# Kernel tuning notes

Measured on AMD Instinct MI355X. Metric: run time of the kernel, lower is better.

The kernel has to match this reference:

```python
import jax, jax.numpy as jnp
import numpy as np

N_NODES = 50000

def _gcn_norm(edge_index, num_nodes):
    # PyG gcn_norm with add_self_loops=True, edge_weight=1
    src = jnp.concatenate([edge_index[0], jnp.arange(num_nodes, dtype=edge_index.dtype)])
    dst = jnp.concatenate([edge_index[1], jnp.arange(num_nodes, dtype=edge_index.dtype)])
    deg = jax.ops.segment_sum(jnp.ones(src.shape[0], dtype=jnp.float32), dst, num_segments=num_nodes)
    dis = jnp.where(deg > 0, jax.lax.rsqrt(jnp.maximum(deg, 1e-12)), 0.0)
    norm = dis[src] * dis[dst]  # [E+N]
    return src, dst, norm

def _gcn_layer(x, src, dst, norm, W, b, num_nodes):
    # x' = x @ W^T; out_i = sum_{(j->i)} norm_e * x'_j + b
    xw = x @ W.T                      # [N, h]
    msg = xw[src] * norm[:, None]     # [E+N, h] gathered + scaled messages
    out = jax.ops.segment_sum(msg, dst, num_segments=num_nodes)
    return out + b

def setup_inputs() -> dict:
    key = jax.random.key(0)
    k1, k2, k3, k4 = jax.random.split(key, 4)
    h = 128
    E = 600000
    embeddings = jax.random.normal(k1, (N_NODES, h), dtype=jnp.float32)
    edge_index = jax.random.randint(k2, (2, E), 0, N_NODES, dtype=jnp.int64)
    scale = 1.0 / np.sqrt(h)
    W1 = jax.random.normal(k3, (h, h), dtype=jnp.float32) * scale
    W2 = jax.random.normal(k4, (h, h), dtype=jnp.float32) * scale
    b1 = jnp.zeros((h,), dtype=jnp.float32)
    b2 = jnp.zeros((h,), dtype=jnp.float32)
    return {"embeddings": embeddings, "edge_index": edge_index,
            "W1": W1, "b1": b1, "W2": W2, "b2": b2}

def reference(embeddings, edge_index, W1, b1, W2, b2):
    src, dst, norm = _gcn_norm(edge_index, N_NODES)
    x = _gcn_layer(embeddings, src, dst, norm, W1, b1, N_NODES)
    x = _gcn_layer(x, src, dst, norm, W2, b2, N_NODES)
    return x
```

## Files before the change

kernel.cpp:

```cpp
#include <hip/hip_runtime.h>

typedef unsigned short u16;
typedef unsigned int   u32;

#define H    128
#define PAD  64
#define LROW 136
#define MT   16

typedef __attribute__((ext_vector_type(8))) short bf16x8;
typedef __attribute__((ext_vector_type(4))) float f32x4;

__device__ __forceinline__ float bfbits2f(u32 bits16) {
  union { float f; u32 u; } c; c.u = bits16 << 16; return c.f;
}
__device__ __forceinline__ u16 f2bf(float f) {
  union { float f; u32 u; } c; c.f = f;
  u32 u = c.u;
  return (u16)((u + 0x7fffu + ((u >> 16) & 1u)) >> 16);
}
__device__ __forceinline__ u32 fbits(float f) {
  union { float f; u32 u; } c; c.f = f; return c.u;
}

__device__ __forceinline__ void acc8(float* a, uint4 v) {
  a[0] += bfbits2f(v.x & 0xffffu); a[1] += bfbits2f(v.x >> 16);
  a[2] += bfbits2f(v.y & 0xffffu); a[3] += bfbits2f(v.y >> 16);
  a[4] += bfbits2f(v.z & 0xffffu); a[5] += bfbits2f(v.z >> 16);
  a[6] += bfbits2f(v.w & 0xffffu); a[7] += bfbits2f(v.w >> 16);
}

__global__ void k_init(int* __restrict__ cnt, int N,
                       const float* __restrict__ W1, u16* __restrict__ W1h, u16* __restrict__ W1l,
                       const float* __restrict__ W2, u16* __restrict__ W2h, u16* __restrict__ W2l) {
  int i = blockIdx.x * blockDim.x + threadIdx.x;
  if (i < N) cnt[i] = 0;
  if (i < H * H) {
    float w1 = W1[i];
    u16 h1 = f2bf(w1);
    W1h[i] = h1; W1l[i] = f2bf(w1 - bfbits2f(h1));
    float w2 = W2[i];
    u16 h2 = f2bf(w2);
    W2h[i] = h2; W2l[i] = f2bf(w2 - bfbits2f(h2));
  }
}

__global__ void k_scatter(const int* __restrict__ srcA, const int* __restrict__ dstA,
                          int* __restrict__ cnt, u16* __restrict__ slot, int E, int N) {
  int e = blockIdx.x * blockDim.x + threadIdx.x;
  if (e < E) {
    int s = srcA[e], d = dstA[e];
    s = s < 0 ? 0 : (s >= N ? N - 1 : s);
    d = d < 0 ? 0 : (d >= N ? N - 1 : d);
    int pos = atomicAdd(&cnt[d], 1);
    if (pos < PAD) slot[(size_t)d * PAD + pos] = (u16)s;
  }
}

__global__ __launch_bounds__(256) void k_prep_x(
    const float2* __restrict__ x, const int* __restrict__ cnt,
    float* __restrict__ dis, u32* __restrict__ xs, u16* __restrict__ slot, int n) {
  int lane = threadIdx.x & 63;
  int node = blockIdx.x * 4 + (threadIdx.x >> 6);
  if (node > n) return;
  if (node == n) {
    xs[(size_t)n * 64 + lane] = 0u;
    return;
  }
  int cv = cnt[node];
  float d = rsqrtf((float)(cv + 1));
  if (lane == 0) dis[node] = d;
  float2 v = x[(size_t)node * 64 + lane];
  xs[(size_t)node * 64 + lane] = (u32)f2bf(d * v.x) | ((u32)f2bf(d * v.y) << 16);
  int cc = cv > PAD ? PAD : cv;
  int ru = (cc + 15) & ~15; ru = ru > PAD ? PAD : ru;
  if (lane >= cc && lane < ru) slot[(size_t)node * PAD + lane] = (u16)n;
}

template <bool BF16OUT>
__global__ __launch_bounds__(256) void k_layer(
    const u32* __restrict__ xs, const int* __restrict__ cntp,
    const u16* __restrict__ slot, const float* __restrict__ dis,
    const u16* __restrict__ Wh, const u16* __restrict__ Wl,
    const float* __restrict__ bias, void* __restrict__ outv, int n) {
  __shared__ u16 lyh[MT * LROW];
  __shared__ u16 lyl[MT * LROW];
  int wv = threadIdx.x >> 6;
  int lane = threadIdx.x & 63;
  int mBase = blockIdx.x * MT;
  int r = lane & 15, q = lane >> 4;
  int h4 = q;
  int c = r;

  int n0 = mBase + wv * 4;
  int slotreg[4];
  int cnts[4];
#pragma unroll
  for (int k = 0; k < 4; ++k) {
    int nk = n0 + k; nk = nk < n ? nk : n - 1;
    slotreg[k] = (int)slot[(size_t)nk * PAD + lane];
    cnts[k] = cntp[nk];
  }
#pragma unroll
  for (int k = 0; k < 4; ++k) {
    int node = n0 + k;
    if (node >= n) break;
    int row = wv * 4 + k;
    int cnt = cnts[k]; cnt = cnt > PAD ? PAD : cnt;
    int quads_p = ((cnt + 15) >> 4) << 2;
    float A[8] = {0.f,0.f,0.f,0.f,0.f,0.f,0.f,0.f};
    if (h4 == 0) {
      uint4 v = *(const uint4*)(xs + (size_t)node * 64 + c * 4);
      acc8(A, v);
    }
    for (int j = 0; j < quads_p; j += 4) {
      int s0 = __shfl(slotreg[k], 4 * j + h4, 64);
      int s1 = __shfl(slotreg[k], 4 * j + 4 + h4, 64);
      int s2 = __shfl(slotreg[k], 4 * j + 8 + h4, 64);
      int s3 = __shfl(slotreg[k], 4 * j + 12 + h4, 64);
      uint4 v0 = *(const uint4*)(xs + (size_t)s0 * 64 + c * 4);
      uint4 v1 = *(const uint4*)(xs + (size_t)s1 * 64 + c * 4);
      uint4 v2 = *(const uint4*)(xs + (size_t)s2 * 64 + c * 4);
      uint4 v3 = *(const uint4*)(xs + (size_t)s3 * 64 + c * 4);
      acc8(A, v0);
      acc8(A, v1);
      acc8(A, v2);
      acc8(A, v3);
    }
#pragma unroll
    for (int kk = 0; kk < 8; ++kk) {
      A[kk] += __shfl(A[kk], lane ^ 16, 64);
      A[kk] += __shfl(A[kk], lane ^ 32, 64);
    }
    float dd = dis[node];
    u32 u[8];
#pragma unroll
    for (int kk = 0; kk < 8; ++kk) { A[kk] *= dd; u[kk] = fbits(A[kk]); }
    if (h4 == 0) {
      uint4 o;
      o.x = (u[0] >> 16) | (u[1] & 0xffff0000u);
      o.y = (u[2] >> 16) | (u[3] & 0xffff0000u);
      o.z = (u[4] >> 16) | (u[5] & 0xffff0000u);
      o.w = (u[6] >> 16) | (u[7] & 0xffff0000u);
      *(uint4*)&lyh[row * LROW + c * 8] = o;
    } else if (h4 == 1) {
      u32 l[8];
#pragma unroll
      for (int kk = 0; kk < 8; ++kk) l[kk] = fbits(A[kk] - bfbits2f(u[kk] >> 16));
      uint4 o;
      o.x = (l[0] >> 16) | (l[1] & 0xffff0000u);
      o.y = (l[2] >> 16) | (l[3] & 0xffff0000u);
      o.z = (l[4] >> 16) | (l[5] & 0xffff0000u);
      o.w = (l[6] >> 16) | (l[7] & 0xffff0000u);
      *(uint4*)&lyl[row * LROW + c * 8] = o;
    }
  }
  __syncthreads();

  bf16x8 Bh[2][4], Bl[2][4];
#pragma unroll
  for (int tt = 0; tt < 2; ++tt) {
    int t = wv * 2 + tt;
#pragma unroll
    for (int ks = 0; ks < 4; ++ks) {
      size_t boff = (size_t)(t * 16 + r) * H + ks * 32 + q * 8;
      Bh[tt][ks] = *(const bf16x8*)(Wh + boff);
      Bl[tt][ks] = *(const bf16x8*)(Wl + boff);
    }
  }
  float bias0 = bias[wv * 32 + r];
  float bias1 = bias[wv * 32 + 16 + r];
  {
    int m0 = mBase;
    bf16x8 Ah[4], Al[4];
#pragma unroll
    for (int ks = 0; ks < 4; ++ks) {
      int off = r * LROW + ks * 32 + q * 8;
      Ah[ks] = *(const bf16x8*)&lyh[off];
      Al[ks] = *(const bf16x8*)&lyl[off];
    }
    f32x4 acc0 = (f32x4){0.f, 0.f, 0.f, 0.f};
    f32x4 acc1 = (f32x4){0.f, 0.f, 0.f, 0.f};
#pragma unroll
    for (int ks = 0; ks < 4; ++ks) {
      acc0 = __builtin_amdgcn_mfma_f32_16x16x32_bf16(Ah[ks], Bh[0][ks], acc0, 0, 0, 0);
      acc1 = __builtin_amdgcn_mfma_f32_16x16x32_bf16(Ah[ks], Bh[1][ks], acc1, 0, 0, 0);
      acc0 = __builtin_amdgcn_mfma_f32_16x16x32_bf16(Al[ks], Bh[0][ks], acc0, 0, 0, 0);
      acc1 = __builtin_amdgcn_mfma_f32_16x16x32_bf16(Al[ks], Bh[1][ks], acc1, 0, 0, 0);
      acc0 = __builtin_amdgcn_mfma_f32_16x16x32_bf16(Ah[ks], Bl[0][ks], acc0, 0, 0, 0);
      acc1 = __builtin_amdgcn_mfma_f32_16x16x32_bf16(Ah[ks], Bl[1][ks], acc1, 0, 0, 0);
    }
    int col0 = wv * 32 + r;
#pragma unroll
    for (int g = 0; g < 4; ++g) {
      int row = m0 + q * 4 + g;
      if (row < n) {
        float v0 = acc0[g] + bias0;
        float v1 = acc1[g] + bias1;
        if (BF16OUT) {
          float dd = dis[row];
          ((u16*)outv)[(size_t)row * H + col0]      = f2bf(dd * v0);
          ((u16*)outv)[(size_t)row * H + col0 + 16] = f2bf(dd * v1);
        } else {
          ((float*)outv)[(size_t)row * H + col0]      = v0;
          ((float*)outv)[(size_t)row * H + col0 + 16] = v1;
        }
      }
    }
  }
}

extern "C" void kernel_launch(void* const* d_in, const int* in_sizes, int n_in,
                              void* d_out, int out_size, void* d_ws, size_t ws_size,
                              hipStream_t stream) {
  const float* x0 = (const float*)d_in[0];
  const int*   ei = (const int*)d_in[1];
  const float* W1 = (const float*)d_in[2];
  const float* b1 = (const float*)d_in[3];
  const float* W2 = (const float*)d_in[4];
  const float* b2 = (const float*)d_in[5];
  int N = in_sizes[0] / H;
  int E = in_sizes[1] / 2;
  const int* srcA = ei;
  const int* dstA = ei + E;

  char* w = (char*)d_ws;
  auto alloc = [&](size_t bytes) -> void* {
    void* p = (void*)w; w += (bytes + 255) & ~(size_t)255; return p;
  };
  int*   cnt  = (int*)  alloc((size_t)N * 4);
  float* dis  = (float*)alloc((size_t)N * 4);
  u16*   slot = (u16*)  alloc((size_t)N * PAD * 2);
  u32*   xs   = (u32*)  alloc((size_t)(N + 1) * 64 * 4);
  u32*   xs2  = (u32*)  alloc((size_t)(N + 1) * 64 * 4);
  u16*   W1h  = (u16*)  alloc((size_t)H * H * 2);
  u16*   W1l  = (u16*)  alloc((size_t)H * H * 2);
  u16*   W2h  = (u16*)  alloc((size_t)H * H * 2);
  u16*   W2l  = (u16*)  alloc((size_t)H * H * 2);

  k_init   <<<(N + 255) / 256, 256, 0, stream>>>(cnt, N, W1, W1h, W1l, W2, W2h, W2l);
  k_scatter<<<(E + 255) / 256, 256, 0, stream>>>(srcA, dstA, cnt, slot, E, N);
  k_prep_x <<<(N + 4) / 4, 256, 0, stream>>>((const float2*)x0, cnt, dis, xs, slot, N);

  hipMemsetAsync((void*)(xs2 + (size_t)N * 64), 0, 64 * 4, stream);
  k_layer<true><<<(N + MT - 1) / MT, 256, 0, stream>>>(
      xs, cnt, slot, dis, W1h, W1l, b1, (void*)xs2, N);
  k_layer<false><<<(N + MT - 1) / MT, 256, 0, stream>>>(
      xs2, cnt, slot, dis, W2h, W2l, b2, d_out, N);
}
```

Measured before the change: 212.4 us.

## Gather neighbor rows with one full wave per row instead of quarter-wave 16B loads

Restructures the aggregation loop so that each lane owns two features and the whole wave reads a single 256-byte neighbor row with 4-byte loads. Slot indices are broadcast with readlane, and 16 loads are issued per batch. This removes the four-way split of lanes across neighbors and the cross-lane shuffle reduction at the end. The cost is narrower per-lane loads, more load instructions per neighbor, and scalar readlane for every neighbor.

```diff
diff --git a/kernel.cpp b/kernel.cpp
--- a/kernel.cpp
+++ b/kernel.cpp
@@ -21,13 +21,6 @@
 }
 __device__ __forceinline__ u32 fbits(float f) {
   union { float f; u32 u; } c; c.f = f; return c.u;
-}
-
-__device__ __forceinline__ void acc8(float* a, uint4 v) {
-  a[0] += bfbits2f(v.x & 0xffffu); a[1] += bfbits2f(v.x >> 16);
-  a[2] += bfbits2f(v.y & 0xffffu); a[3] += bfbits2f(v.y >> 16);
-  a[4] += bfbits2f(v.z & 0xffffu); a[5] += bfbits2f(v.z >> 16);
-  a[6] += bfbits2f(v.w & 0xffffu); a[7] += bfbits2f(v.w >> 16);
 }
 
 __global__ void k_init(int* __restrict__ cnt, int N,
@@ -89,8 +82,6 @@
   int lane = threadIdx.x & 63;
   int mBase = blockIdx.x * MT;
   int r = lane & 15, q = lane >> 4;
-  int h4 = q;
-  int c = r;
 
   int n0 = mBase + wv * 4;
   int slotreg[4];
@@ -107,53 +98,30 @@
     if (node >= n) break;
     int row = wv * 4 + k;
     int cnt = cnts[k]; cnt = cnt > PAD ? PAD : cnt;
-    int quads_p = ((cnt + 15) >> 4) << 2;
-    float A[8] = {0.f,0.f,0.f,0.f,0.f,0.f,0.f,0.f};
-    if (h4 == 0) {
-      uint4 v = *(const uint4*)(xs + (size_t)node * 64 + c * 4);
-      acc8(A, v);
-    }
-    for (int j = 0; j < quads_p; j += 4) {
-      int s0 = __shfl(slotreg[k], 4 * j + h4, 64);
-      int s1 = __shfl(slotreg[k], 4 * j + 4 + h4, 64);
-      int s2 = __shfl(slotreg[k], 4 * j + 8 + h4, 64);
-      int s3 = __shfl(slotreg[k], 4 * j + 12 + h4, 64);
-      uint4 v0 = *(const uint4*)(xs + (size_t)s0 * 64 + c * 4);
-      uint4 v1 = *(const uint4*)(xs + (size_t)s1 * 64 + c * 4);
-      uint4 v2 = *(const uint4*)(xs + (size_t)s2 * 64 + c * 4);
-      uint4 v3 = *(const uint4*)(xs + (size_t)s3 * 64 + c * 4);
-      acc8(A, v0);
-      acc8(A, v1);
-      acc8(A, v2);
-      acc8(A, v3);
-    }
-#pragma unroll
-    for (int kk = 0; kk < 8; ++kk) {
-      A[kk] += __shfl(A[kk], lane ^ 16, 64);
-      A[kk] += __shfl(A[kk], lane ^ 32, 64);
+    int nb = (cnt + 15) >> 4;
+    u32 self = xs[(size_t)node * 64 + lane];
+    float a0 = bfbits2f(self & 0xffffu);
+    float a1 = bfbits2f(self >> 16);
+    for (int b = 0; b < nb; ++b) {
+      u32 v[16];
+#pragma unroll
+      for (int t = 0; t < 16; ++t) {
+        int s = __builtin_amdgcn_readlane((u32)slotreg[k], (u32)(b * 16 + t));
+        v[t] = xs[(size_t)(s & 0xffff) * 64 + lane];
+      }
+#pragma unroll
+      for (int t = 0; t < 16; ++t) {
+        a0 += bfbits2f(v[t] & 0xffffu);
+        a1 += bfbits2f(v[t] >> 16);
+      }
     }
     float dd = dis[node];
-    u32 u[8];
-#pragma unroll
-    for (int kk = 0; kk < 8; ++kk) { A[kk] *= dd; u[kk] = fbits(A[kk]); }
-    if (h4 == 0) {
-      uint4 o;
-      o.x = (u[0] >> 16) | (u[1] & 0xffff0000u);
-      o.y = (u[2] >> 16) | (u[3] & 0xffff0000u);
-      o.z = (u[4] >> 16) | (u[5] & 0xffff0000u);
-      o.w = (u[6] >> 16) | (u[7] & 0xffff0000u);
-      *(uint4*)&lyh[row * LROW + c * 8] = o;
-    } else if (h4 == 1) {
-      u32 l[8];
-#pragma unroll
-      for (int kk = 0; kk < 8; ++kk) l[kk] = fbits(A[kk] - bfbits2f(u[kk] >> 16));
-      uint4 o;
-      o.x = (l[0] >> 16) | (l[1] & 0xffff0000u);
-      o.y = (l[2] >> 16) | (l[3] & 0xffff0000u);
-      o.z = (l[4] >> 16) | (l[5] & 0xffff0000u);
-      o.w = (l[6] >> 16) | (l[7] & 0xffff0000u);
-      *(uint4*)&lyl[row * LROW + c * 8] = o;
-    }
+    a0 *= dd; a1 *= dd;
+    u32 u0 = fbits(a0), u1 = fbits(a1);
+    *(u32*)&lyh[row * LROW + lane * 2] = (u0 >> 16) | (u1 & 0xffff0000u);
+    u32 l0 = fbits(a0 - bfbits2f(u0 >> 16));
+    u32 l1 = fbits(a1 - bfbits2f(u1 >> 16));
+    *(u32*)&lyl[row * LROW + lane * 2] = (l0 >> 16) | (l1 & 0xffff0000u);
   }
   __syncthreads();
 
@@ -241,8 +209,8 @@
   k_init   <<<(N + 255) / 256, 256, 0, stream>>>(cnt, N, W1, W1h, W1l, W2, W2h, W2l);
   k_scatter<<<(E + 255) / 256, 256, 0, stream>>>(srcA, dstA, cnt, slot, E, N);
   k_prep_x <<<(N + 4) / 4, 256, 0, stream>>>((const float2*)x0, cnt, dis, xs, slot, N);
-
   hipMemsetAsync((void*)(xs2 + (size_t)N * 64), 0, 64 * 4, stream);
+
   k_layer<true><<<(N + MT - 1) / MT, 256, 0, stream>>>(
       xs, cnt, slot, dis, W1h, W1l, b1, (void*)xs2, N);
   k_layer<false><<<(N + MT - 1) / MT, 256, 0, stream>>>(
```

New measurement: 213.2 us. Within noise of the previous version (+0.4%).

## Aggregate four nodes per wave concurrently, one node per 16-lane quarter

Applied to the files above, without the earlier changes.

The neighbour gather in k_layer now assigns each 16-lane quarter of a wave to its own node, instead of processing the wave's four nodes one after another with the quarters splitting a single node's edges. This removes the cross-quarter shuffle reductions and the serial per-node loop. The loop trip count is the maximum degree among the four nodes, so the quarters with lighter nodes gather padded sentinel slots, which is why prep now fills all remaining slots with the sentinel. The separate memset for the xs2 zero row is folded into the prep kernel, saving one launch.

```diff
diff --git a/kernel.cpp b/kernel.cpp
--- a/kernel.cpp
+++ b/kernel.cpp
@@ -59,12 +59,14 @@
 
 __global__ __launch_bounds__(256) void k_prep_x(
     const float2* __restrict__ x, const int* __restrict__ cnt,
-    float* __restrict__ dis, u32* __restrict__ xs, u16* __restrict__ slot, int n) {
+    float* __restrict__ dis, u32* __restrict__ xs, u32* __restrict__ xs2,
+    u16* __restrict__ slot, int n) {
   int lane = threadIdx.x & 63;
   int node = blockIdx.x * 4 + (threadIdx.x >> 6);
   if (node > n) return;
   if (node == n) {
-    xs[(size_t)n * 64 + lane] = 0u;
+    xs [(size_t)n * 64 + lane] = 0u;
+    xs2[(size_t)n * 64 + lane] = 0u;
     return;
   }
   int cv = cnt[node];
@@ -73,8 +75,7 @@
   float2 v = x[(size_t)node * 64 + lane];
   xs[(size_t)node * 64 + lane] = (u32)f2bf(d * v.x) | ((u32)f2bf(d * v.y) << 16);
   int cc = cv > PAD ? PAD : cv;
-  int ru = (cc + 15) & ~15; ru = ru > PAD ? PAD : ru;
-  if (lane >= cc && lane < ru) slot[(size_t)node * PAD + lane] = (u16)n;
+  if (lane >= cc) slot[(size_t)node * PAD + lane] = (u16)n;
 }
 
 template <bool BF16OUT>
@@ -89,35 +90,32 @@
   int lane = threadIdx.x & 63;
   int mBase = blockIdx.x * MT;
   int r = lane & 15, q = lane >> 4;
-  int h4 = q;
-  int c = r;
 
   int n0 = mBase + wv * 4;
-  int slotreg[4];
-  int cnts[4];
-#pragma unroll
-  for (int k = 0; k < 4; ++k) {
-    int nk = n0 + k; nk = nk < n ? nk : n - 1;
-    slotreg[k] = (int)slot[(size_t)nk * PAD + lane];
-    cnts[k] = cntp[nk];
-  }
-#pragma unroll
-  for (int k = 0; k < 4; ++k) {
-    int node = n0 + k;
-    if (node >= n) break;
-    int row = wv * 4 + k;
-    int cnt = cnts[k]; cnt = cnt > PAD ? PAD : cnt;
-    int quads_p = ((cnt + 15) >> 4) << 2;
-    float A[8] = {0.f,0.f,0.f,0.f,0.f,0.f,0.f,0.f};
-    if (h4 == 0) {
-      uint4 v = *(const uint4*)(xs + (size_t)node * 64 + c * 4);
-      acc8(A, v);
-    }
-    for (int j = 0; j < quads_p; j += 4) {
-      int s0 = __shfl(slotreg[k], 4 * j + h4, 64);
-      int s1 = __shfl(slotreg[k], 4 * j + 4 + h4, 64);
-      int s2 = __shfl(slotreg[k], 4 * j + 8 + h4, 64);
-      int s3 = __shfl(slotreg[k], 4 * j + 12 + h4, 64);
+  int qb = lane & 48;
+  int c  = r;
+  int nq = n0 + q; nq = nq < n ? nq : n - 1;
+  int sreg[4];
+#pragma unroll
+  for (int b = 0; b < 4; ++b)
+    sreg[b] = (int)slot[(size_t)nq * PAD + b * 16 + c];
+  int cq = cntp[nq]; cq = cq > PAD ? PAD : cq;
+  int m1 = __shfl(cq, lane ^ 16, 64); int t1 = cq > m1 ? cq : m1;
+  int m2 = __shfl(t1, lane ^ 32, 64); int tmax = t1 > m2 ? t1 : m2;
+
+  float A[8] = {0.f,0.f,0.f,0.f,0.f,0.f,0.f,0.f};
+  uint4 sv = *(const uint4*)(xs + (size_t)nq * 64 + c * 4);
+  acc8(A, sv);
+#pragma unroll
+  for (int b = 0; b < 4; ++b) {
+    if (b * 16 >= tmax) break;
+    int jend = tmax - b * 16; jend = jend > 16 ? 16 : jend;
+    int sr = sreg[b];
+    for (int j = 0; j < jend; j += 4) {
+      int s0 = __shfl(sr, qb + j + 0, 64);
+      int s1 = __shfl(sr, qb + j + 1, 64);
+      int s2 = __shfl(sr, qb + j + 2, 64);
+      int s3 = __shfl(sr, qb + j + 3, 64);
       uint4 v0 = *(const uint4*)(xs + (size_t)s0 * 64 + c * 4);
       uint4 v1 = *(const uint4*)(xs + (size_t)s1 * 64 + c * 4);
       uint4 v2 = *(const uint4*)(xs + (size_t)s2 * 64 + c * 4);
@@ -127,33 +125,27 @@
       acc8(A, v2);
       acc8(A, v3);
     }
-#pragma unroll
-    for (int kk = 0; kk < 8; ++kk) {
-      A[kk] += __shfl(A[kk], lane ^ 16, 64);
-      A[kk] += __shfl(A[kk], lane ^ 32, 64);
-    }
-    float dd = dis[node];
+  }
+  {
+    float dd = dis[nq];
     u32 u[8];
 #pragma unroll
-    for (int kk = 0; kk < 8; ++kk) { A[kk] *= dd; u[kk] = fbits(A[kk]); }
-    if (h4 == 0) {
-      uint4 o;
-      o.x = (u[0] >> 16) | (u[1] & 0xffff0000u);
-      o.y = (u[2] >> 16) | (u[3] & 0xffff0000u);
-      o.z = (u[4] >> 16) | (u[5] & 0xffff0000u);
-      o.w = (u[6] >> 16) | (u[7] & 0xffff0000u);
-      *(uint4*)&lyh[row * LROW + c * 8] = o;
-    } else if (h4 == 1) {
-      u32 l[8];
-#pragma unroll
-      for (int kk = 0; kk < 8; ++kk) l[kk] = fbits(A[kk] - bfbits2f(u[kk] >> 16));
-      uint4 o;
-      o.x = (l[0] >> 16) | (l[1] & 0xffff0000u);
-      o.y = (l[2] >> 16) | (l[3] & 0xffff0000u);
-      o.z = (l[4] >> 16) | (l[5] & 0xffff0000u);
-      o.w = (l[6] >> 16) | (l[7] & 0xffff0000u);
-      *(uint4*)&lyl[row * LROW + c * 8] = o;
-    }
+    for (int k = 0; k < 8; ++k) { A[k] *= dd; u[k] = fbits(A[k]); }
+    uint4 oh, ol;
+    oh.x = (u[0] >> 16) | (u[1] & 0xffff0000u);
+    oh.y = (u[2] >> 16) | (u[3] & 0xffff0000u);
+    oh.z = (u[4] >> 16) | (u[5] & 0xffff0000u);
+    oh.w = (u[6] >> 16) | (u[7] & 0xffff0000u);
+    u32 l[8];
+#pragma unroll
+    for (int k = 0; k < 8; ++k) l[k] = fbits(A[k] - bfbits2f(u[k] >> 16));
+    ol.x = (l[0] >> 16) | (l[1] & 0xffff0000u);
+    ol.y = (l[2] >> 16) | (l[3] & 0xffff0000u);
+    ol.z = (l[4] >> 16) | (l[5] & 0xffff0000u);
+    ol.w = (l[6] >> 16) | (l[7] & 0xffff0000u);
+    int lrow = wv * 4 + q;
+    *(uint4*)&lyh[lrow * LROW + c * 8] = oh;
+    *(uint4*)&lyl[lrow * LROW + c * 8] = ol;
   }
   __syncthreads();
 
@@ -171,7 +163,6 @@
   float bias0 = bias[wv * 32 + r];
   float bias1 = bias[wv * 32 + 16 + r];
   {
-    int m0 = mBase;
     bf16x8 Ah[4], Al[4];
 #pragma unroll
     for (int ks = 0; ks < 4; ++ks) {
@@ -193,7 +184,7 @@
     int col0 = wv * 32 + r;
 #pragma unroll
     for (int g = 0; g < 4; ++g) {
-      int row = m0 + q * 4 + g;
+      int row = mBase + q * 4 + g;
       if (row < n) {
         float v0 = acc0[g] + bias0;
         float v1 = acc1[g] + bias1;
@@ -240,9 +231,8 @@
 
   k_init   <<<(N + 255) / 256, 256, 0, stream>>>(cnt, N, W1, W1h, W1l, W2, W2h, W2l);
   k_scatter<<<(E + 255) / 256, 256, 0, stream>>>(srcA, dstA, cnt, slot, E, N);
-  k_prep_x <<<(N + 4) / 4, 256, 0, stream>>>((const float2*)x0, cnt, dis, xs, slot, N);
-
-  hipMemsetAsync((void*)(xs2 + (size_t)N * 64), 0, 64 * 4, stream);
+  k_prep_x <<<(N + 4) / 4, 256, 0, stream>>>((const float2*)x0, cnt, dis, xs, xs2, slot, N);
+
   k_layer<true><<<(N + MT - 1) / MT, 256, 0, stream>>>(
       xs, cnt, slot, dis, W1h, W1l, b1, (void*)xs2, N);
   k_layer<false><<<(N + MT - 1) / MT, 256, 0, stream>>>(
```

Result: faster. 206.7 us (-2.7%).
